# Kernel optimization log

Measured on AMD Instinct MI355X. Metric: run time of the kernel, lower is better.

Reference implementation:

```python
import jax, jax.numpy as jnp
import numpy as np

B, T, E, H = 4, 2048, 4096, 128

def setup_inputs() -> dict:
    key = jax.random.key(0)
    ks = jax.random.split(key, 5)
    x = jax.random.normal(ks[0], (B, T, E), dtype=jnp.float32)
    pos_emb = jax.random.normal(ks[1], (B, T, E), dtype=jnp.float32)
    # torch nn.Linear(E, H, bias=False) weights have shape [H, E]
    scale = 1.0 / np.sqrt(E)
    Wq = jax.random.normal(ks[2], (H, E), dtype=jnp.float32) * scale
    Wk = jax.random.normal(ks[3], (H, E), dtype=jnp.float32) * scale
    Wv = jax.random.normal(ks[4], (H, E), dtype=jnp.float32) * scale
    return {"x": x, "pos_emb": pos_emb, "Wq": Wq, "Wk": Wk, "Wv": Wv}

def reference(x, pos_emb, Wq, Wk, Wv):
    Bd, Td, Ed = x.shape
    q = jnp.einsum('bte,he->bth', x, Wq)        # [B,T,H]
    k = jnp.einsum('bte,he->bth', pos_emb, Wk)  # [B,T,H] (key is computed from pos_emb, per source)
    v = jnp.einsum('bte,he->bth', x, Wv)        # [B,T,H]
    # NOTE: source scales by full model dim E**-0.5, not head_size**-0.5
    scores = jnp.einsum('bqh,bkh->bqk', q, k) * (Ed ** -0.5)  # [B,T,T]
    causal = jnp.tril(jnp.ones((Td, Td), dtype=bool))
    scores = jnp.where(causal[None, :, :], scores, -jnp.inf)
    attn = jax.nn.softmax(scores, axis=-1)
    out = jnp.einsum('bqk,bkh->bqh', attn, v)   # [B,T,H]
    return out
```

## Files before the change

kernel.cpp:

```cpp
#include <hip/hip_runtime.h>

#define BB 4
#define TT 2048
#define EE 4096
#define HH 128
#define MM (BB*TT)
#define SCALE 0.015625f

typedef short short8 __attribute__((ext_vector_type(8)));
typedef float f32x4 __attribute__((ext_vector_type(4)));
typedef unsigned short ushort_t;
typedef unsigned int u32;

__device__ __forceinline__ unsigned short f2bf(float x) {
    unsigned int u = __float_as_uint(x);
    u = (u + 0x7fffu + ((u >> 16) & 1u)) >> 16;
    return (unsigned short)u;
}

__device__ __forceinline__ void gl_lds16(const ushort_t* g, ushort_t* l) {
    __builtin_amdgcn_global_load_lds(
        (const __attribute__((address_space(1))) u32*)(g),
        (__attribute__((address_space(3))) u32*)(l), 16, 0, 0);
}

__global__ __launch_bounds__(256) void wconv(
    const float* __restrict__ Wq, const float* __restrict__ Wk,
    const float* __restrict__ Wv, ushort_t* __restrict__ Wb)
{
    const int gid = blockIdx.x * 256 + threadIdx.x;
    const int which = gid >> 16;
    const int rem = gid & 65535;
    const float* W = (which == 0) ? Wq : (which == 1) ? Wk : Wv;
    const float sc = (which == 0) ? SCALE : 1.0f;
    const float4 f0 = *(const float4*)(W + (size_t)rem * 8);
    const float4 f1 = *(const float4*)(W + (size_t)rem * 8 + 4);
    short8 pk;
    pk[0] = (short)f2bf(f0.x * sc); pk[1] = (short)f2bf(f0.y * sc);
    pk[2] = (short)f2bf(f0.z * sc); pk[3] = (short)f2bf(f0.w * sc);
    pk[4] = (short)f2bf(f1.x * sc); pk[5] = (short)f2bf(f1.y * sc);
    pk[6] = (short)f2bf(f1.z * sc); pk[7] = (short)f2bf(f1.w * sc);
    *(short8*)(Wb + (size_t)which * 524288 + (size_t)rem * 8) = pk;
}

#define KSPLIT 4
#define KSPAN  1024
#define KSTEP  64
#define NSTEPS 16
#define ASTRIDE 72

__global__ __launch_bounds__(256) void proj_mfma(
    const float* __restrict__ x, const float* __restrict__ pe,
    const ushort_t* __restrict__ Wb, float* __restrict__ Pp)
{
    const int mb   = blockIdx.x;
    const int widx = blockIdx.y;
    const int sp   = blockIdx.z;
    const float* in = (widx == 1) ? pe : x;
    const ushort_t* W = Wb + (size_t)widx * (128 * EE);

    const int rb    = mb * 128;
    const int kbase = sp * KSPAN;

    const int tid  = threadIdx.x;
    const int lane = tid & 63, wave = tid >> 6;
    const int wr = wave & 1, wc = wave >> 1;
    const int fr = lane & 15, quad = lane >> 4, ko = quad * 8;

    __shared__ __align__(16) ushort_t Asl[128 * ASTRIDE];
    __shared__ __align__(16) ushort_t Bsl[2][128 * KSTEP];

    f32x4 acc[4][4];
    #pragma unroll
    for (int m = 0; m < 4; m++)
        #pragma unroll
        for (int n = 0; n < 4; n++) acc[m][n] = (f32x4){0.f,0.f,0.f,0.f};

    const int arow = tid >> 1;
    const int acol = (tid & 1) * 32;
    const float* aptr = in + (size_t)(rb + arow) * EE + kbase + acol;

    const ushort_t* bsrc = W + (size_t)(tid >> 3) * EE + kbase + (tid & 7) * 8;
    const int bdst = tid * 8;

    float4 ar[8];

#define LOAD_A(KOFS) do { \
    const float* p_ = aptr + (KOFS); \
    _Pragma("unroll") \
    for (int j = 0; j < 8; j++) ar[j] = *(const float4*)(p_ + j * 4); \
} while (0)

#define STAGE_B(KOFS, BUF) do { \
    _Pragma("unroll") \
    for (int j = 0; j < 4; j++) \
        gl_lds16(bsrc + (KOFS) + (size_t)j * 32 * EE, \
                 &Bsl[BUF][bdst + j * 2048]); \
} while (0)

#define WRITE_A() do { \
    _Pragma("unroll") \
    for (int j = 0; j < 4; j++) { \
        short8 s_; \
        const float4 a0_ = ar[2*j], a1_ = ar[2*j+1]; \
        s_[0]=(short)f2bf(a0_.x); s_[1]=(short)f2bf(a0_.y); \
        s_[2]=(short)f2bf(a0_.z); s_[3]=(short)f2bf(a0_.w); \
        s_[4]=(short)f2bf(a1_.x); s_[5]=(short)f2bf(a1_.y); \
        s_[6]=(short)f2bf(a1_.z); s_[7]=(short)f2bf(a1_.w); \
        *(short8*)&Asl[arow * ASTRIDE + acol + j * 8] = s_; \
    } \
} while (0)

    LOAD_A(0);
    STAGE_B(0, 0);
    WRITE_A();
    __syncthreads();

    for (int s = 0; s < NSTEPS; s++) {
        const int buf = s & 1;
        const bool more = (s + 1 < NSTEPS);
        if (more) {
            LOAD_A((s + 1) * KSTEP);
            STAGE_B((s + 1) * KSTEP, buf ^ 1);
        }
        #pragma unroll
        for (int h = 0; h < 2; h++) {
            short8 af[4], bf_[4];
            #pragma unroll
            for (int m = 0; m < 4; m++)
                af[m] = *(short8*)&Asl[(wr*64 + m*16 + fr) * ASTRIDE + h*32 + ko];
            #pragma unroll
            for (int n = 0; n < 4; n++)
                bf_[n] = *(short8*)&Bsl[buf][(wc*64 + n*16 + fr) * KSTEP + h*32 + ko];
            #pragma unroll
            for (int m = 0; m < 4; m++)
                #pragma unroll
                for (int n = 0; n < 4; n++)
                    acc[m][n] = __builtin_amdgcn_mfma_f32_16x16x32_bf16(
                        af[m], bf_[n], acc[m][n], 0, 0, 0);
        }
        __syncthreads();
        if (more) {
            WRITE_A();
            __syncthreads();
        }
    }

    float* P = Pp + ((size_t)(widx * KSPLIT + sp) * MM + rb) * HH;
    #pragma unroll
    for (int m = 0; m < 4; m++)
        #pragma unroll
        for (int n = 0; n < 4; n++)
            #pragma unroll
            for (int r = 0; r < 4; r++)
                P[(size_t)(wr*64 + m*16 + quad*4 + r) * HH
                  + wc*64 + n*16 + fr] = acc[m][n][r];

#undef LOAD_A
#undef STAGE_B
#undef WRITE_A
}

__global__ __launch_bounds__(256) void projcomb(
    const float* __restrict__ Pp,
    ushort_t* __restrict__ qo, ushort_t* __restrict__ ko_,
    ushort_t* __restrict__ vto)
{
    const int mb   = blockIdx.x;
    const int widx = blockIdx.y;
    const int tid  = threadIdx.x;
    const int m0 = mb * 64;
    const int r_ = tid >> 2;
    const int h0 = (tid & 3) * 32;

    __shared__ ushort_t T[128 * 72];

    const float* base = Pp + ((size_t)widx * KSPLIT * MM + m0 + r_) * HH + h0;
    float accv[32];
    #pragma unroll
    for (int j = 0; j < 8; j++) {
        float4 a = *(const float4*)(base + j * 4);
        accv[4*j+0] = a.x; accv[4*j+1] = a.y; accv[4*j+2] = a.z; accv[4*j+3] = a.w;
    }
    #pragma unroll
    for (int s = 1; s < KSPLIT; s++) {
        const float* bs = base + (size_t)s * MM * HH;
        #pragma unroll
        for (int j = 0; j < 8; j++) {
            float4 a = *(const float4*)(bs + j * 4);
            accv[4*j+0] += a.x; accv[4*j+1] += a.y;
            accv[4*j+2] += a.z; accv[4*j+3] += a.w;
        }
    }

    if (widx < 2) {
        ushort_t* out = (widx == 0) ? qo : ko_;
        #pragma unroll
        for (int j = 0; j < 4; j++) {
            short8 s_;
            #pragma unroll
            for (int e = 0; e < 8; e++) s_[e] = (short)f2bf(accv[j*8 + e]);
            *(short8*)&out[(size_t)(m0 + r_) * HH + h0 + j * 8] = s_;
        }
    } else {
        #pragma unroll
        for (int e = 0; e < 32; e++)
            T[(h0 + e) * 72 + r_] = f2bf(accv[e]);
        __syncthreads();
        const int h = tid >> 1, ms = (tid & 1) * 32;
        #pragma unroll
        for (int j = 0; j < 4; j++)
            *(short8*)&vto[(size_t)h * MM + m0 + ms + j * 8]
                = *(short8*)&T[h * 72 + ms + j * 8];
    }
}

__global__ __launch_bounds__(256) void attn_mfma(
    const ushort_t* __restrict__ qb, const ushort_t* __restrict__ kbf,
    const ushort_t* __restrict__ vtb,
    float* __restrict__ OP, float* __restrict__ LP)
{
    const int b = blockIdx.z;
    const int s = blockIdx.y;
    const int t = 63 - (int)blockIdx.x;
    const int tid  = threadIdx.x;
    const int lane = tid & 63, wave = tid >> 6;
    const int fr = lane & 15, quad = lane >> 4, ko = quad * 8;

    const int q0 = t * 32;
    const int C  = (t + 2) >> 1;
    const int cs = (C + 1) >> 1;
    const int c0 = s ? cs : 0;
    const int c1 = s ? C  : cs;

    __shared__ __align__(16) ushort_t Qs[32 * 136];
    __shared__ __align__(16) ushort_t Ks[64 * 136];
    __shared__ __align__(16) ushort_t Vt[128 * 72];
    __shared__ __align__(16) ushort_t Ps[32 * 72];
    __shared__ float lred[2][32];

    for (int f = tid; f < 512; f += 256) {
        const int row = f >> 4, sg = f & 15;
        *(short8*)&Qs[row * 136 + sg * 8] =
            *(const short8*)(qb + (size_t)(b * TT + q0 + row) * HH + sg * 8);
    }

    const int rhS = (wave & 1) * 16, cqS = (wave >> 1) * 32;
    const int rhO = (wave & 1) * 16, chO = (wave >> 1) * 64;

    f32x4 oacc[4];
    #pragma unroll
    for (int i = 0; i < 4; i++) oacc[i] = (f32x4){0.f,0.f,0.f,0.f};
    float lacc[4] = {0.f, 0.f, 0.f, 0.f};

    for (int c = c0; c < c1; c++) {
        const int kb_ = c * 64;
        for (int f = tid; f < 1024; f += 256) {
            const int row = f >> 4, sg = f & 15;
            *(short8*)&Ks[row * 136 + sg * 8] =
                *(const short8*)(kbf + (size_t)(b * TT + kb_ + row) * HH + sg * 8);
        }
        for (int f = tid; f < 1024; f += 256) {
            const int h = f >> 3, sg = f & 7;
            *(short8*)&Vt[h * 72 + sg * 8] =
                *(const short8*)(vtb + (size_t)h * MM + b * TT + kb_ + sg * 8);
        }
        __syncthreads();

        f32x4 sacc[2];
        sacc[0] = (f32x4){0.f,0.f,0.f,0.f};
        sacc[1] = (f32x4){0.f,0.f,0.f,0.f};
        #pragma unroll
        for (int kk = 0; kk < 128; kk += 32) {
            const short8 af = *(short8*)&Qs[(rhS + fr) * 136 + kk + ko];
            const short8 b0 = *(short8*)&Ks[(cqS + fr) * 136 + kk + ko];
            const short8 b1 = *(short8*)&Ks[(cqS + 16 + fr) * 136 + kk + ko];
            sacc[0] = __builtin_amdgcn_mfma_f32_16x16x32_bf16(af, b0, sacc[0], 0, 0, 0);
            sacc[1] = __builtin_amdgcn_mfma_f32_16x16x32_bf16(af, b1, sacc[1], 0, 0, 0);
        }

        #pragma unroll
        for (int tl = 0; tl < 2; tl++)
            #pragma unroll
            for (int r = 0; r < 4; r++) {
                const int row = rhS + quad * 4 + r;
                const int col = cqS + tl * 16 + fr;
                const float p = ((kb_ + col) <= (q0 + row)) ? __expf(sacc[tl][r]) : 0.f;
                lacc[r] += p;
                Ps[row * 72 + col] = f2bf(p);
            }
        __syncthreads();

        #pragma unroll
        for (int ks = 0; ks < 64; ks += 32) {
            const short8 af = *(short8*)&Ps[(rhO + fr) * 72 + ks + ko];
            #pragma unroll
            for (int tl = 0; tl < 4; tl++) {
                const short8 bf_ = *(short8*)&Vt[(chO + tl * 16 + fr) * 72 + ks + ko];
                oacc[tl] = __builtin_amdgcn_mfma_f32_16x16x32_bf16(af, bf_, oacc[tl], 0, 0, 0);
            }
        }
        __syncthreads();
    }

    #pragma unroll
    for (int r = 0; r < 4; r++) {
        float v = lacc[r];
        #pragma unroll
        for (int m = 1; m < 16; m <<= 1) v += __shfl_xor(v, m);
        lacc[r] = v;
    }
    if (fr == 0) {
        #pragma unroll
        for (int r = 0; r < 4; r++)
            lred[wave >> 1][rhS + quad * 4 + r] = lacc[r];
    }
    __syncthreads();
    const int pbase = ((b * 64 + t) * 2 + s);
    if (tid < 32) LP[(size_t)pbase * 32 + tid] = lred[0][tid] + lred[1][tid];

    #pragma unroll
    for (int tl = 0; tl < 4; tl++)
        #pragma unroll
        for (int r = 0; r < 4; r++) {
            const int row = rhO + quad * 4 + r;
            const int col = chO + tl * 16 + fr;
            OP[(size_t)pbase * 4096 + row * 128 + col] = oacc[tl][r];
        }
}

__global__ __launch_bounds__(256) void combine(
    const float* __restrict__ OP, const float* __restrict__ LP,
    float* __restrict__ out)
{
    const int gid = blockIdx.x * 256 + threadIdx.x;
    const int b = gid >> 16;
    const int rem = gid & 65535;
    const int qrow = rem >> 5, h4 = rem & 31;
    const int t = qrow >> 5, r = qrow & 31;
    const int base = (b * 64 + t) * 2;
    const float l = LP[(size_t)base * 32 + r] + LP[(size_t)(base + 1) * 32 + r];
    const float inv = 1.f / l;
    const float4 a = ((const float4*)OP)[(size_t)base * 1024 + r * 32 + h4];
    const float4 c = ((const float4*)OP)[(size_t)(base + 1) * 1024 + r * 32 + h4];
    float4 res;
    res.x = (a.x + c.x) * inv; res.y = (a.y + c.y) * inv;
    res.z = (a.z + c.z) * inv; res.w = (a.w + c.w) * inv;
    ((float4*)out)[gid] = res;
}

extern "C" void kernel_launch(void* const* d_in, const int* in_sizes, int n_in,
                              void* d_out, int out_size, void* d_ws, size_t ws_size,
                              hipStream_t stream) {
    const float* x  = (const float*)d_in[0];
    const float* pe = (const float*)d_in[1];
    const float* Wq = (const float*)d_in[2];
    const float* Wk = (const float*)d_in[3];
    const float* Wv = (const float*)d_in[4];
    float* out = (float*)d_out;

    ushort_t* qb  = (ushort_t*)d_ws;
    ushort_t* kbf = qb  + (size_t)MM * HH;
    ushort_t* vtb = kbf + (size_t)MM * HH;
    ushort_t* Wb  = vtb + (size_t)MM * HH;
    float* Pp = (float*)(Wb + (size_t)3 * 128 * 4096);
    float* OP = Pp;
    float* LP = OP + (size_t)512 * 4096;

    wconv    <<<768, 256, 0, stream>>>(Wq, Wk, Wv, Wb);
    proj_mfma<<<dim3(64, 3, KSPLIT), 256, 0, stream>>>(x, pe, Wb, Pp);
    projcomb <<<dim3(128, 3), 256, 0, stream>>>(Pp, qb, kbf, vtb);
    attn_mfma<<<dim3(64, 2, BB), 256, 0, stream>>>(qb, kbf, vtb, OP, LP);
    combine  <<<1024, 256, 0, stream>>>(OP, LP, out);
}
```

Baseline: 402.8 us.

## Replace LDS-staged projection GEMM with register-direct per-wave MFMA loads

The projection kernel no longer stages tiles of x and the weights in shared memory. Each wave now owns 32 rows and loads its A fragments (fp32, converted to bf16 in registers) and B fragments straight from global memory into MFMA operands. This drops the LDS traffic, the barriers and the double buffering, and the launch bounds now request 3 blocks per CU. The cost is that the four waves in a block each reload the full weight tile with no sharing, and global loads are no longer overlapped with compute by an explicit pipeline.

```diff
diff --git a/kernel.cpp b/kernel.cpp
--- a/kernel.cpp
+++ b/kernel.cpp
@@ -16,12 +16,6 @@
     unsigned int u = __float_as_uint(x);
     u = (u + 0x7fffu + ((u >> 16) & 1u)) >> 16;
     return (unsigned short)u;
-}
-
-__device__ __forceinline__ void gl_lds16(const ushort_t* g, ushort_t* l) {
-    __builtin_amdgcn_global_load_lds(
-        (const __attribute__((address_space(1))) u32*)(g),
-        (__attribute__((address_space(3))) u32*)(l), 16, 0, 0);
 }
 
 __global__ __launch_bounds__(256) void wconv(
@@ -45,11 +39,8 @@
 
 #define KSPLIT 4
 #define KSPAN  1024
-#define KSTEP  64
-#define NSTEPS 16
-#define ASTRIDE 72
-
-__global__ __launch_bounds__(256) void proj_mfma(
+
+__global__ __launch_bounds__(256, 3) void proj_mfma(
     const float* __restrict__ x, const float* __restrict__ pe,
     const ushort_t* __restrict__ Wb, float* __restrict__ Pp)
 {
@@ -59,106 +50,58 @@
     const float* in = (widx == 1) ? pe : x;
     const ushort_t* W = Wb + (size_t)widx * (128 * EE);
 
-    const int rb    = mb * 128;
-    const int kbase = sp * KSPAN;
-
     const int tid  = threadIdx.x;
     const int lane = tid & 63, wave = tid >> 6;
-    const int wr = wave & 1, wc = wave >> 1;
-    const int fr = lane & 15, quad = lane >> 4, ko = quad * 8;
-
-    __shared__ __align__(16) ushort_t Asl[128 * ASTRIDE];
-    __shared__ __align__(16) ushort_t Bsl[2][128 * KSTEP];
-
-    f32x4 acc[4][4];
-    #pragma unroll
-    for (int m = 0; m < 4; m++)
-        #pragma unroll
-        for (int n = 0; n < 4; n++) acc[m][n] = (f32x4){0.f,0.f,0.f,0.f};
-
-    const int arow = tid >> 1;
-    const int acol = (tid & 1) * 32;
-    const float* aptr = in + (size_t)(rb + arow) * EE + kbase + acol;
-
-    const ushort_t* bsrc = W + (size_t)(tid >> 3) * EE + kbase + (tid & 7) * 8;
-    const int bdst = tid * 8;
-
-    float4 ar[8];
-
-#define LOAD_A(KOFS) do { \
-    const float* p_ = aptr + (KOFS); \
-    _Pragma("unroll") \
-    for (int j = 0; j < 8; j++) ar[j] = *(const float4*)(p_ + j * 4); \
-} while (0)
-
-#define STAGE_B(KOFS, BUF) do { \
-    _Pragma("unroll") \
-    for (int j = 0; j < 4; j++) \
-        gl_lds16(bsrc + (KOFS) + (size_t)j * 32 * EE, \
-                 &Bsl[BUF][bdst + j * 2048]); \
-} while (0)
-
-#define WRITE_A() do { \
-    _Pragma("unroll") \
-    for (int j = 0; j < 4; j++) { \
-        short8 s_; \
-        const float4 a0_ = ar[2*j], a1_ = ar[2*j+1]; \
-        s_[0]=(short)f2bf(a0_.x); s_[1]=(short)f2bf(a0_.y); \
-        s_[2]=(short)f2bf(a0_.z); s_[3]=(short)f2bf(a0_.w); \
-        s_[4]=(short)f2bf(a1_.x); s_[5]=(short)f2bf(a1_.y); \
-        s_[6]=(short)f2bf(a1_.z); s_[7]=(short)f2bf(a1_.w); \
-        *(short8*)&Asl[arow * ASTRIDE + acol + j * 8] = s_; \
-    } \
-} while (0)
-
-    LOAD_A(0);
-    STAGE_B(0, 0);
-    WRITE_A();
-    __syncthreads();
-
-    for (int s = 0; s < NSTEPS; s++) {
-        const int buf = s & 1;
-        const bool more = (s + 1 < NSTEPS);
-        if (more) {
-            LOAD_A((s + 1) * KSTEP);
-            STAGE_B((s + 1) * KSTEP, buf ^ 1);
-        }
-        #pragma unroll
-        for (int h = 0; h < 2; h++) {
-            short8 af[4], bf_[4];
-            #pragma unroll
-            for (int m = 0; m < 4; m++)
-                af[m] = *(short8*)&Asl[(wr*64 + m*16 + fr) * ASTRIDE + h*32 + ko];
-            #pragma unroll
-            for (int n = 0; n < 4; n++)
-                bf_[n] = *(short8*)&Bsl[buf][(wc*64 + n*16 + fr) * KSTEP + h*32 + ko];
-            #pragma unroll
-            for (int m = 0; m < 4; m++)
-                #pragma unroll
-                for (int n = 0; n < 4; n++)
-                    acc[m][n] = __builtin_amdgcn_mfma_f32_16x16x32_bf16(
-                        af[m], bf_[n], acc[m][n], 0, 0, 0);
-        }
-        __syncthreads();
-        if (more) {
-            WRITE_A();
-            __syncthreads();
+    const int fr = lane & 15, quad = lane >> 4;
+
+    const int rb    = mb * 128 + wave * 32;
+    const int kbase = sp * KSPAN;
+
+    f32x4 acc[2][8];
+    #pragma unroll
+    for (int m = 0; m < 2; m++)
+        #pragma unroll
+        for (int n = 0; n < 8; n++) acc[m][n] = (f32x4){0.f,0.f,0.f,0.f};
+
+    const float* a0p = in + (size_t)(rb + fr) * EE + kbase + quad * 8;
+    const float* a1p = in + (size_t)(rb + 16 + fr) * EE + kbase + quad * 8;
+    const ushort_t* bp = W + (size_t)fr * EE + kbase + quad * 8;
+
+    for (int kk = 0; kk < KSPAN; kk += 32) {
+        const float4 x00 = *(const float4*)(a0p + kk);
+        const float4 x01 = *(const float4*)(a0p + kk + 4);
+        const float4 x10 = *(const float4*)(a1p + kk);
+        const float4 x11 = *(const float4*)(a1p + kk + 4);
+        short8 bf[8];
+        #pragma unroll
+        for (int n = 0; n < 8; n++)
+            bf[n] = *(const short8*)(bp + (size_t)n * 16 * EE + kk);
+
+        short8 af0, af1;
+        af0[0]=(short)f2bf(x00.x); af0[1]=(short)f2bf(x00.y);
+        af0[2]=(short)f2bf(x00.z); af0[3]=(short)f2bf(x00.w);
+        af0[4]=(short)f2bf(x01.x); af0[5]=(short)f2bf(x01.y);
+        af0[6]=(short)f2bf(x01.z); af0[7]=(short)f2bf(x01.w);
+        af1[0]=(short)f2bf(x10.x); af1[1]=(short)f2bf(x10.y);
+        af1[2]=(short)f2bf(x10.z); af1[3]=(short)f2bf(x10.w);
+        af1[4]=(short)f2bf(x11.x); af1[5]=(short)f2bf(x11.y);
+        af1[6]=(short)f2bf(x11.z); af1[7]=(short)f2bf(x11.w);
+
+        #pragma unroll
+        for (int n = 0; n < 8; n++) {
+            acc[0][n] = __builtin_amdgcn_mfma_f32_16x16x32_bf16(af0, bf[n], acc[0][n], 0, 0, 0);
+            acc[1][n] = __builtin_amdgcn_mfma_f32_16x16x32_bf16(af1, bf[n], acc[1][n], 0, 0, 0);
         }
     }
 
     float* P = Pp + ((size_t)(widx * KSPLIT + sp) * MM + rb) * HH;
     #pragma unroll
-    for (int m = 0; m < 4; m++)
-        #pragma unroll
-        for (int n = 0; n < 4; n++)
+    for (int m = 0; m < 2; m++)
+        #pragma unroll
+        for (int n = 0; n < 8; n++)
             #pragma unroll
             for (int r = 0; r < 4; r++)
-                P[(size_t)(wr*64 + m*16 + quad*4 + r) * HH
-                  + wc*64 + n*16 + fr] = acc[m][n][r];
-
-#undef LOAD_A
-#undef STAGE_B
-#undef WRITE_A
+                P[(size_t)(m * 16 + quad * 4 + r) * HH + n * 16 + fr] = acc[m][n][r];
 }
 
 __global__ __launch_bounds__(256) void projcomb(
```

Result: slower. 420.1 us (+4.3%).
